# Kernel tuning notes

Measured on AMD Instinct MI355X. Metric: run time of the kernel, lower is better.

## Reference

```python
import jax, jax.numpy as jnp
import numpy as np

T, B, D = 2048, 32, 1024
AH, H = 128, 8
N, N2 = D // H, AH // H


def setup_inputs() -> dict:
    key = jax.random.key(0)
    ks = jax.random.split(key, 7)
    s1 = 1.0 / np.sqrt(N)
    s2 = 1.0 / np.sqrt(N2)
    return {
        "hyp": jax.random.normal(ks[0], (T, B, D), dtype=jnp.float32),
        "W_w": jax.random.uniform(ks[1], (N2, N), jnp.float32, -s1, s1),
        "W_b": jax.random.uniform(ks[2], (N2,), jnp.float32, -s1, s1),
        "Wm_w": jax.random.uniform(ks[3], (N2, N), jnp.float32, -s1, s1),
        "Wm_b": jax.random.uniform(ks[4], (N2,), jnp.float32, -s1, s1),
        "Wh_w": jax.random.uniform(ks[5], (1, N2), jnp.float32, -s2, s2),
        "Wh_b": jax.random.uniform(ks[6], (1,), jnp.float32, -s2, s2),
        "dan_hidden_size": D,
        "attention_hidden_size": AH,
        "multihead_size": H,
    }


def reference(hyp, W_w, W_b, Wm_w, Wm_b, Wh_w, Wh_b,
              dan_hidden_size, attention_hidden_size, multihead_size):
    t, b, d = hyp.shape
    h_ = multihead_size
    n = d // h_
    # (T,B,D) -> (B,H,T,N); weights are shared across heads in the original loop
    x = jnp.transpose(hyp.reshape(t, b, h_, n), (1, 2, 0, 3))
    m = x.mean(axis=2, keepdims=True)                      # (B,H,1,N) mean over time
    gate_x = jnp.tanh(jnp.einsum('bhtn,kn->bhtk', x, W_w) + W_b)
    gate_m = jnp.tanh(jnp.einsum('bhtn,kn->bhtk', m, Wm_w) + Wm_b)
    hgate = gate_x * gate_m                                 # (B,H,T,N2)
    logits = jnp.einsum('bhtk,ok->bhto', hgate, Wh_w) + Wh_b  # (B,H,T,1)
    a = jax.nn.softmax(logits, axis=2)                      # softmax over time
    c = jnp.sum(a * x, axis=2)                              # (B,H,N)
    return c.reshape(b, h_ * n)
```

## Files before the change

kernel.cpp:

```cpp
#include <hip/hip_runtime.h>
#include <hip/hip_fp16.h>
#include <math.h>

#define T_   2048
#define B_   32
#define D_   1024
#define H_   8
#define N_   128
#define NK   16
#define TSPL 8
#define TBLK (T_/TSPL)
#define BD4  (B_*D_/4)
#define APS  132
#define LOG2E 1.4426950408889634f

typedef __attribute__((ext_vector_type(8))) _Float16 half8;
typedef __attribute__((ext_vector_type(4))) float f32x4;

__device__ __forceinline__ half8 to_half8(float4 a, float4 b) {
    half8 r;
    r[0] = (_Float16)a.x; r[1] = (_Float16)a.y;
    r[2] = (_Float16)a.z; r[3] = (_Float16)a.w;
    r[4] = (_Float16)b.x; r[5] = (_Float16)b.y;
    r[6] = (_Float16)b.z; r[7] = (_Float16)b.w;
    return r;
}

__device__ __forceinline__ float tanh_fast(float d) {
    return 1.f - 2.f * __frcp_rn(exp2f(d * (2.f * LOG2E)) + 1.f);
}

#define LOADX(dst, step_) { \
    const int trow_ = t0 + (step_) * 64 + w * 16 + kk; \
    const size_t rb_ = (size_t)trow_ * BD4 + base4; \
    (dst)[0] = hyp4[rb_ + g * 2];      (dst)[1] = hyp4[rb_ + g * 2 + 1]; \
    (dst)[2] = hyp4[rb_ + 8 + g * 2];  (dst)[3] = hyp4[rb_ + 8 + g * 2 + 1]; \
    (dst)[4] = hyp4[rb_ + 16 + g * 2]; (dst)[5] = hyp4[rb_ + 16 + g * 2 + 1]; \
    (dst)[6] = hyp4[rb_ + 24 + g * 2]; (dst)[7] = hyp4[rb_ + 24 + g * 2 + 1]; }

__global__ __launch_bounds__(256, 4) void k_p(const float* __restrict__ hyp,
                                              const float* __restrict__ Ww,
                                              const float* __restrict__ Wb,
                                              float* __restrict__ part,
                                              __half* __restrict__ Pbuf) {
    __shared__ float red[4 * N_];
    __shared__ __half Pl[TBLK * NK];
    const int tid  = threadIdx.x;
    const int lane = tid & 63;
    const int w    = tid >> 6;
    const int blk  = blockIdx.x;
    const int bh   = blk >> 3;
    const int spl  = blk & 7;
    const int b = bh >> 3, h = bh & 7;
    const int t0 = spl * TBLK;
    const float4* hyp4 = (const float4*)hyp;
    const float4* Ww4  = (const float4*)Ww;
    const int base4 = b * (D_ / 4) + h * (N_ / 4);
    const int kk = lane & 15;
    const int g  = lane >> 4;

    half8 wf[4];
#pragma unroll
    for (int ks = 0; ks < 4; ++ks) {
        float4 wa  = Ww4[kk * 32 + ks * 8 + g * 2];
        float4 wb4 = Ww4[kk * 32 + ks * 8 + g * 2 + 1];
        wf[ks] = to_half8(wa, wb4);
    }
    const float wbr = Wb[kk];

    float4 cs[8];
#pragma unroll
    for (int m = 0; m < 8; ++m) cs[m] = make_float4(0.f, 0.f, 0.f, 0.f);

#pragma unroll
    for (int step = 0; step < 4; ++step) {
        float4 xq[8];
        LOADX(xq, step);
#pragma unroll
        for (int m = 0; m < 8; ++m) {
            cs[m].x += xq[m].x; cs[m].y += xq[m].y;
            cs[m].z += xq[m].z; cs[m].w += xq[m].w;
        }
        f32x4 acc = {0.f, 0.f, 0.f, 0.f};
#pragma unroll
        for (int ks = 0; ks < 4; ++ks) {
            half8 xf = to_half8(xq[2*ks], xq[2*ks+1]);
            acc = __builtin_amdgcn_mfma_f32_16x16x32_f16(xf, wf[ks], acc, 0, 0, 0);
        }
        const int tl = step * 64 + w * 16 + g * 4;
#pragma unroll
        for (int i = 0; i < 4; ++i)
            Pl[(tl + i) * NK + kk] = __float2half(tanh_fast(acc[i] + wbr));
    }
    __syncthreads();
    {
        const uint4* src = (const uint4*)Pl;
        uint4* dst = (uint4*)(Pbuf + ((size_t)bh * T_ + t0) * NK);
        dst[tid]       = src[tid];
        dst[tid + 256] = src[tid + 256];
    }
#pragma unroll
    for (int m = 0; m < 8; ++m) {
#pragma unroll
        for (int mask = 1; mask <= 8; mask <<= 1) {
            cs[m].x += __shfl_xor(cs[m].x, mask, 64);
            cs[m].y += __shfl_xor(cs[m].y, mask, 64);
            cs[m].z += __shfl_xor(cs[m].z, mask, 64);
            cs[m].w += __shfl_xor(cs[m].w, mask, 64);
        }
    }
    if (kk == 0) {
#pragma unroll
        for (int m = 0; m < 8; ++m) {
            int nb = 32 * (m >> 1) + 8 * g + 4 * (m & 1);
            red[w * N_ + nb + 0] = cs[m].x;
            red[w * N_ + nb + 1] = cs[m].y;
            red[w * N_ + nb + 2] = cs[m].z;
            red[w * N_ + nb + 3] = cs[m].w;
        }
    }
    __syncthreads();
    if (tid < N_)
        part[blk * N_ + tid] = (red[tid] + red[N_ + tid])
                             + (red[2*N_ + tid] + red[3*N_ + tid]);
}

__global__ __launch_bounds__(256, 4) void k_att(const float* __restrict__ hyp,
                                                const float* __restrict__ part,
                                                const float* __restrict__ Wmw,
                                                const float* __restrict__ Wmb,
                                                const float* __restrict__ Whw,
                                                const __half* __restrict__ Pbuf,
                                                float* __restrict__ attp) {
    __shared__ float m_l[N_];
    __shared__ float gw_l[NK];
    __shared__ float wexp_l[TBLK];
    __shared__ float4 red4[8][32];
    __shared__ float zred[4];
    const int tid  = threadIdx.x;
    const int lane = tid & 63;
    const int w    = tid >> 6;
    const int j    = (int)blockIdx.x;
    const int blk  = (j & 7) + 8 * (255 - (j >> 3));
    const int bh   = blk >> 3;
    const int spl  = blk & 7;
    const int b = bh >> 3, h = bh & 7;
    const int t0 = spl * TBLK;
    const float4* hyp4 = (const float4*)hyp;
    const int base4 = b * (D_ / 4) + h * (N_ / 4);

    if (tid < N_) {
        float s = 0.f;
#pragma unroll
        for (int s8 = 0; s8 < TSPL; ++s8) s += part[(bh * TSPL + s8) * N_ + tid];
        m_l[tid] = s * (1.f / (float)T_);
    }
    __syncthreads();
    if (tid < N_) {
        int k = tid >> 3, g3 = tid & 7;
        float dsum = 0.f;
#pragma unroll
        for (int i = 0; i < 16; ++i) {
            int n = g3 * 16 + i;
            dsum = fmaf(m_l[n], Wmw[k * N_ + n], dsum);
        }
        dsum += __shfl_xor(dsum, 1, 64);
        dsum += __shfl_xor(dsum, 2, 64);
        dsum += __shfl_xor(dsum, 4, 64);
        if (g3 == 0) gw_l[k] = tanhf(dsum + Wmb[k]) * Whw[k];
    }
    __syncthreads();

    {
        const uint4* pv = (const uint4*)(Pbuf + ((size_t)bh * T_ + t0) * NK);
        union { uint4 u; __half2 hh[4]; } Pa, Pb;
        Pa.u = pv[2 * tid];
        Pb.u = pv[2 * tid + 1];
        float lg = 0.f;
#pragma unroll
        for (int q = 0; q < 4; ++q) {
            float2 f0 = __half22float2(Pa.hh[q]);
            float2 f1 = __half22float2(Pb.hh[q]);
            lg = fmaf(f0.x, gw_l[2*q + 0], lg);
            lg = fmaf(f0.y, gw_l[2*q + 1], lg);
            lg = fmaf(f1.x, gw_l[8 + 2*q + 0], lg);
            lg = fmaf(f1.y, gw_l[8 + 2*q + 1], lg);
        }
        float e = exp2f(lg * LOG2E);
        wexp_l[tid] = e;
        float z = e;
        z += __shfl_xor(z, 1, 64);  z += __shfl_xor(z, 2, 64);
        z += __shfl_xor(z, 4, 64);  z += __shfl_xor(z, 8, 64);
        z += __shfl_xor(z, 16, 64); z += __shfl_xor(z, 32, 64);
        if (lane == 0) zred[w] = z;
    }
    __syncthreads();

    const int col4 = tid & 31, tg = tid >> 5;
    float4 c0 = {0.f,0.f,0.f,0.f}, c1 = {0.f,0.f,0.f,0.f};
    const float* we = &wexp_l[tg * 32];
    const size_t rbase = (size_t)(t0 + tg * 32) * BD4 + base4 + col4;
#pragma unroll
    for (int i = 0; i < 32; i += 2) {
        float w0 = we[i], w1 = we[i + 1];
        float4 x0 = hyp4[rbase + (size_t)i * BD4];
        float4 x1 = hyp4[rbase + (size_t)(i + 1) * BD4];
        c0.x = fmaf(w0, x0.x, c0.x); c0.y = fmaf(w0, x0.y, c0.y);
        c0.z = fmaf(w0, x0.z, c0.z); c0.w = fmaf(w0, x0.w, c0.w);
        c1.x = fmaf(w1, x1.x, c1.x); c1.y = fmaf(w1, x1.y, c1.y);
        c1.z = fmaf(w1, x1.z, c1.z); c1.w = fmaf(w1, x1.w, c1.w);
    }
    c0.x += c1.x; c0.y += c1.y; c0.z += c1.z; c0.w += c1.w;
    red4[tg][col4] = c0;
    __syncthreads();
    if (tid < 32) {
        float4 s = {0.f,0.f,0.f,0.f};
#pragma unroll
        for (int gg = 0; gg < 8; ++gg) {
            float4 v = red4[gg][tid];
            s.x += v.x; s.y += v.y; s.z += v.z; s.w += v.w;
        }
        *(float4*)&attp[(size_t)blk * APS + tid * 4] = s;
    } else if (tid == 32) {
        attp[(size_t)blk * APS + N_] =
            (zred[0] + zred[1]) + (zred[2] + zred[3]);
    }
}

__global__ __launch_bounds__(128) void k_red(const float* __restrict__ attp,
                                             float* __restrict__ out) {
    int bh = blockIdx.x, tid = threadIdx.x;
    float Z = 0.f, c = 0.f;
#pragma unroll
    for (int s = 0; s < TSPL; ++s) {
        const float* pp = &attp[(size_t)(bh * TSPL + s) * APS];
        Z += pp[N_];
        c += pp[tid];
    }
    out[bh * N_ + tid] = c / Z;
}

extern "C" void kernel_launch(void* const* d_in, const int* in_sizes, int n_in,
                              void* d_out, int out_size, void* d_ws, size_t ws_size,
                              hipStream_t stream) {
    const float* hyp = (const float*)d_in[0];
    const float* Ww  = (const float*)d_in[1];
    const float* Wb  = (const float*)d_in[2];
    const float* Wmw = (const float*)d_in[3];
    const float* Wmb = (const float*)d_in[4];
    const float* Whw = (const float*)d_in[5];
    float* out  = (float*)d_out;
    float* part = (float*)d_ws;
    float* attp = part + 2048 * N_;
    __half* Pbuf = (__half*)((char*)d_ws + (4 << 20));

    k_p  <<<dim3(B_ * H_ * TSPL), 256, 0, stream>>>(hyp, Ww, Wb, part, Pbuf);
    k_att<<<dim3(B_ * H_ * TSPL), 256, 0, stream>>>(hyp, part, Wmw, Wmb, Whw,
                                                    Pbuf, attp);
    k_red<<<dim3(B_ * H_), 128, 0, stream>>>(attp, out);
}
```

Baseline: 108.1 us.

## Stash fp16 copy of x in k_p and read it in attention pass

While streaming hyp, the projection kernel now writes an fp16 copy of each head's x rows into workspace, laid out contiguously per (b,h). The attention kernel reads that half-size copy for the weighted sum instead of re-reading the fp32 input. The hyp loads become nontemporal, and the reversed block order that favoured cache reuse is removed. This trades a second full fp32 read for a half-size write plus a half-size read, and it lowers the precision of the weighted sum of x.

```diff
diff --git a/kernel.cpp b/kernel.cpp
--- a/kernel.cpp
+++ b/kernel.cpp
@@ -17,7 +17,7 @@
 typedef __attribute__((ext_vector_type(8))) _Float16 half8;
 typedef __attribute__((ext_vector_type(4))) float f32x4;
 
-__device__ __forceinline__ half8 to_half8(float4 a, float4 b) {
+__device__ __forceinline__ half8 to_half8(f32x4 a, f32x4 b) {
     half8 r;
     r[0] = (_Float16)a.x; r[1] = (_Float16)a.y;
     r[2] = (_Float16)a.z; r[3] = (_Float16)a.w;
@@ -30,19 +30,24 @@
     return 1.f - 2.f * __frcp_rn(exp2f(d * (2.f * LOG2E)) + 1.f);
 }
 
-#define LOADX(dst, step_) { \
+#define LOADX_NT(dst, step_) { \
     const int trow_ = t0 + (step_) * 64 + w * 16 + kk; \
     const size_t rb_ = (size_t)trow_ * BD4 + base4; \
-    (dst)[0] = hyp4[rb_ + g * 2];      (dst)[1] = hyp4[rb_ + g * 2 + 1]; \
-    (dst)[2] = hyp4[rb_ + 8 + g * 2];  (dst)[3] = hyp4[rb_ + 8 + g * 2 + 1]; \
-    (dst)[4] = hyp4[rb_ + 16 + g * 2]; (dst)[5] = hyp4[rb_ + 16 + g * 2 + 1]; \
-    (dst)[6] = hyp4[rb_ + 24 + g * 2]; (dst)[7] = hyp4[rb_ + 24 + g * 2 + 1]; }
+    (dst)[0] = __builtin_nontemporal_load(&hyp4n[rb_ + g * 2]); \
+    (dst)[1] = __builtin_nontemporal_load(&hyp4n[rb_ + g * 2 + 1]); \
+    (dst)[2] = __builtin_nontemporal_load(&hyp4n[rb_ + 8 + g * 2]); \
+    (dst)[3] = __builtin_nontemporal_load(&hyp4n[rb_ + 8 + g * 2 + 1]); \
+    (dst)[4] = __builtin_nontemporal_load(&hyp4n[rb_ + 16 + g * 2]); \
+    (dst)[5] = __builtin_nontemporal_load(&hyp4n[rb_ + 16 + g * 2 + 1]); \
+    (dst)[6] = __builtin_nontemporal_load(&hyp4n[rb_ + 24 + g * 2]); \
+    (dst)[7] = __builtin_nontemporal_load(&hyp4n[rb_ + 24 + g * 2 + 1]); }
 
 __global__ __launch_bounds__(256, 4) void k_p(const float* __restrict__ hyp,
                                               const float* __restrict__ Ww,
                                               const float* __restrict__ Wb,
                                               float* __restrict__ part,
-                                              __half* __restrict__ Pbuf) {
+                                              __half* __restrict__ Pbuf,
+                                              __half* __restrict__ xcb) {
     __shared__ float red[4 * N_];
     __shared__ __half Pl[TBLK * NK];
     const int tid  = threadIdx.x;
@@ -53,8 +58,8 @@
     const int spl  = blk & 7;
     const int b = bh >> 3, h = bh & 7;
     const int t0 = spl * TBLK;
-    const float4* hyp4 = (const float4*)hyp;
-    const float4* Ww4  = (const float4*)Ww;
+    const f32x4* hyp4n = (const f32x4*)hyp;
+    const f32x4* Ww4   = (const f32x4*)Ww;
     const int base4 = b * (D_ / 4) + h * (N_ / 4);
     const int kk = lane & 15;
     const int g  = lane >> 4;
@@ -62,20 +67,22 @@
     half8 wf[4];
 #pragma unroll
     for (int ks = 0; ks < 4; ++ks) {
-        float4 wa  = Ww4[kk * 32 + ks * 8 + g * 2];
-        float4 wb4 = Ww4[kk * 32 + ks * 8 + g * 2 + 1];
+        f32x4 wa  = Ww4[kk * 32 + ks * 8 + g * 2];
+        f32x4 wb4 = Ww4[kk * 32 + ks * 8 + g * 2 + 1];
         wf[ks] = to_half8(wa, wb4);
     }
     const float wbr = Wb[kk];
 
-    float4 cs[8];
-#pragma unroll
-    for (int m = 0; m < 8; ++m) cs[m] = make_float4(0.f, 0.f, 0.f, 0.f);
+    f32x4 cs[8];
+#pragma unroll
+    for (int m = 0; m < 8; ++m) cs[m] = (f32x4){0.f, 0.f, 0.f, 0.f};
 
 #pragma unroll
     for (int step = 0; step < 4; ++step) {
-        float4 xq[8];
-        LOADX(xq, step);
+        f32x4 xq[8];
+        LOADX_NT(xq, step);
+        const int trow = t0 + step * 64 + w * 16 + kk;
+        __half* xrow = xcb + ((size_t)bh * T_ + trow) * N_;
 #pragma unroll
         for (int m = 0; m < 8; ++m) {
             cs[m].x += xq[m].x; cs[m].y += xq[m].y;
@@ -86,6 +93,7 @@
         for (int ks = 0; ks < 4; ++ks) {
             half8 xf = to_half8(xq[2*ks], xq[2*ks+1]);
             acc = __builtin_amdgcn_mfma_f32_16x16x32_f16(xf, wf[ks], acc, 0, 0, 0);
+            *(half8*)&xrow[ks * 32 + g * 8] = xf;
         }
         const int tl = step * 64 + w * 16 + g * 4;
 #pragma unroll
@@ -125,7 +133,7 @@
                              + (red[2*N_ + tid] + red[3*N_ + tid]);
 }
 
-__global__ __launch_bounds__(256, 4) void k_att(const float* __restrict__ hyp,
+__global__ __launch_bounds__(256, 4) void k_att(const __half* __restrict__ xcb,
                                                 const float* __restrict__ part,
                                                 const float* __restrict__ Wmw,
                                                 const float* __restrict__ Wmb,
@@ -135,19 +143,15 @@
     __shared__ float m_l[N_];
     __shared__ float gw_l[NK];
     __shared__ float wexp_l[TBLK];
-    __shared__ float4 red4[8][32];
+    __shared__ float4 redc[16][16][2];
     __shared__ float zred[4];
     const int tid  = threadIdx.x;
     const int lane = tid & 63;
     const int w    = tid >> 6;
-    const int j    = (int)blockIdx.x;
-    const int blk  = (j & 7) + 8 * (255 - (j >> 3));
+    const int blk  = (int)blockIdx.x;
     const int bh   = blk >> 3;
     const int spl  = blk & 7;
-    const int b = bh >> 3, h = bh & 7;
     const int t0 = spl * TBLK;
-    const float4* hyp4 = (const float4*)hyp;
-    const int base4 = b * (D_ / 4) + h * (N_ / 4);
 
     if (tid < N_) {
         float s = 0.f;
@@ -196,32 +200,37 @@
     }
     __syncthreads();
 
-    const int col4 = tid & 31, tg = tid >> 5;
+    const int c8 = tid & 15, tg = tid >> 4;
     float4 c0 = {0.f,0.f,0.f,0.f}, c1 = {0.f,0.f,0.f,0.f};
-    const float* we = &wexp_l[tg * 32];
-    const size_t rbase = (size_t)(t0 + tg * 32) * BD4 + base4 + col4;
-#pragma unroll
-    for (int i = 0; i < 32; i += 2) {
-        float w0 = we[i], w1 = we[i + 1];
-        float4 x0 = hyp4[rbase + (size_t)i * BD4];
-        float4 x1 = hyp4[rbase + (size_t)(i + 1) * BD4];
-        c0.x = fmaf(w0, x0.x, c0.x); c0.y = fmaf(w0, x0.y, c0.y);
-        c0.z = fmaf(w0, x0.z, c0.z); c0.w = fmaf(w0, x0.w, c0.w);
-        c1.x = fmaf(w1, x1.x, c1.x); c1.y = fmaf(w1, x1.y, c1.y);
-        c1.z = fmaf(w1, x1.z, c1.z); c1.w = fmaf(w1, x1.w, c1.w);
-    }
-    c0.x += c1.x; c0.y += c1.y; c0.z += c1.z; c0.w += c1.w;
-    red4[tg][col4] = c0;
-    __syncthreads();
-    if (tid < 32) {
-        float4 s = {0.f,0.f,0.f,0.f};
-#pragma unroll
-        for (int gg = 0; gg < 8; ++gg) {
-            float4 v = red4[gg][tid];
-            s.x += v.x; s.y += v.y; s.z += v.z; s.w += v.w;
-        }
-        *(float4*)&attp[(size_t)blk * APS + tid * 4] = s;
-    } else if (tid == 32) {
+    const float* we = &wexp_l[tg * 16];
+    const __half* xr = xcb + ((size_t)bh * T_ + t0 + tg * 16) * N_ + c8 * 8;
+#pragma unroll
+    for (int i = 0; i < 16; ++i) {
+        union { uint4 u; __half2 hh[4]; } X;
+        X.u = *(const uint4*)(xr + (size_t)i * N_);
+        float e = we[i];
+        float2 f0 = __half22float2(X.hh[0]);
+        float2 f1 = __half22float2(X.hh[1]);
+        float2 f2 = __half22float2(X.hh[2]);
+        float2 f3 = __half22float2(X.hh[3]);
+        c0.x = fmaf(e, f0.x, c0.x); c0.y = fmaf(e, f0.y, c0.y);
+        c0.z = fmaf(e, f1.x, c0.z); c0.w = fmaf(e, f1.y, c0.w);
+        c1.x = fmaf(e, f2.x, c1.x); c1.y = fmaf(e, f2.y, c1.y);
+        c1.z = fmaf(e, f3.x, c1.z); c1.w = fmaf(e, f3.y, c1.w);
+    }
+    redc[tg][c8][0] = c0;
+    redc[tg][c8][1] = c1;
+    __syncthreads();
+    if (tid < N_) {
+        int cc8 = tid >> 3, jj = tid & 7;
+        float s = 0.f;
+#pragma unroll
+        for (int g16 = 0; g16 < 16; ++g16) {
+            const float* rr = (const float*)&redc[g16][cc8][0];
+            s += rr[jj];
+        }
+        attp[(size_t)blk * APS + tid] = s;
+    } else if (tid == N_) {
         attp[(size_t)blk * APS + N_] =
             (zred[0] + zred[1]) + (zred[2] + zred[3]);
     }
@@ -253,9 +262,11 @@
     float* part = (float*)d_ws;
     float* attp = part + 2048 * N_;
     __half* Pbuf = (__half*)((char*)d_ws + (4 << 20));
-
-    k_p  <<<dim3(B_ * H_ * TSPL), 256, 0, stream>>>(hyp, Ww, Wb, part, Pbuf);
-    k_att<<<dim3(B_ * H_ * TSPL), 256, 0, stream>>>(hyp, part, Wmw, Wmb, Whw,
+    __half* xcb  = (__half*)((char*)d_ws + (24 << 20));
+
+    k_p  <<<dim3(B_ * H_ * TSPL), 256, 0, stream>>>(hyp, Ww, Wb, part, Pbuf,
+                                                    xcb);
+    k_att<<<dim3(B_ * H_ * TSPL), 256, 0, stream>>>(xcb, part, Wmw, Wmb, Whw,
                                                     Pbuf, attp);
     k_red<<<dim3(B_ * H_), 128, 0, stream>>>(attp, out);
 }
```

Result: slower. 143.6 us (+32.8%).

## Fuse three kernels into one 1024-thread block per batch-head

Applied to the files above, without the earlier changes.

Replaces the three-kernel pipeline (partial mean + gate projection, attention, final reduction) with a single kernel in which one 1024-thread block handles a whole (batch, head) pair across all 2048 timesteps. The gate values and softmax weights stay in shared memory, so the global Pbuf and partial-sum round trips and two kernel launches disappear. In exchange the grid shrinks from 2048 blocks to 256, which may underfill the GPU. Each block also needs a large shared-memory footprint, limiting occupancy while the memory-bound second pass over hyp runs.

```diff
diff --git a/kernel.cpp b/kernel.cpp
--- a/kernel.cpp
+++ b/kernel.cpp
@@ -8,16 +8,13 @@
 #define H_   8
 #define N_   128
 #define NK   16
-#define TSPL 8
-#define TBLK (T_/TSPL)
 #define BD4  (B_*D_/4)
-#define APS  132
 #define LOG2E 1.4426950408889634f
 
 typedef __attribute__((ext_vector_type(8))) _Float16 half8;
 typedef __attribute__((ext_vector_type(4))) float f32x4;
 
-__device__ __forceinline__ half8 to_half8(float4 a, float4 b) {
+__device__ __forceinline__ half8 to_half8(f32x4 a, f32x4 b) {
     half8 r;
     r[0] = (_Float16)a.x; r[1] = (_Float16)a.y;
     r[2] = (_Float16)a.z; r[3] = (_Float16)a.w;
@@ -30,31 +27,26 @@
     return 1.f - 2.f * __frcp_rn(exp2f(d * (2.f * LOG2E)) + 1.f);
 }
 
-#define LOADX(dst, step_) { \
-    const int trow_ = t0 + (step_) * 64 + w * 16 + kk; \
-    const size_t rb_ = (size_t)trow_ * BD4 + base4; \
-    (dst)[0] = hyp4[rb_ + g * 2];      (dst)[1] = hyp4[rb_ + g * 2 + 1]; \
-    (dst)[2] = hyp4[rb_ + 8 + g * 2];  (dst)[3] = hyp4[rb_ + 8 + g * 2 + 1]; \
-    (dst)[4] = hyp4[rb_ + 16 + g * 2]; (dst)[5] = hyp4[rb_ + 16 + g * 2 + 1]; \
-    (dst)[6] = hyp4[rb_ + 24 + g * 2]; (dst)[7] = hyp4[rb_ + 24 + g * 2 + 1]; }
-
-__global__ __launch_bounds__(256, 4) void k_p(const float* __restrict__ hyp,
-                                              const float* __restrict__ Ww,
-                                              const float* __restrict__ Wb,
-                                              float* __restrict__ part,
-                                              __half* __restrict__ Pbuf) {
-    __shared__ float red[4 * N_];
-    __shared__ __half Pl[TBLK * NK];
+__global__ __launch_bounds__(1024, 4) void k_fused(
+        const float* __restrict__ hyp,  const float* __restrict__ Ww,
+        const float* __restrict__ Wb,   const float* __restrict__ Wmw,
+        const float* __restrict__ Wmb,  const float* __restrict__ Whw,
+        float* __restrict__ out) {
+    __shared__ __align__(16) __half Pl[T_ * NK];
+    __shared__ __align__(16) float scratch[4096];
+    __shared__ float wexp_l[T_];
+    __shared__ float m_l[N_];
+    __shared__ float gw_l[NK];
+    __shared__ float zred[16];
+    __shared__ float zfin_s;
+
     const int tid  = threadIdx.x;
     const int lane = tid & 63;
     const int w    = tid >> 6;
-    const int blk  = blockIdx.x;
-    const int bh   = blk >> 3;
-    const int spl  = blk & 7;
+    const int bh   = blockIdx.x;
     const int b = bh >> 3, h = bh & 7;
-    const int t0 = spl * TBLK;
-    const float4* hyp4 = (const float4*)hyp;
-    const float4* Ww4  = (const float4*)Ww;
+    const f32x4* hyp4n = (const f32x4*)hyp;
+    const f32x4* Ww4   = (const f32x4*)Ww;
     const int base4 = b * (D_ / 4) + h * (N_ / 4);
     const int kk = lane & 15;
     const int g  = lane >> 4;
@@ -62,20 +54,26 @@
     half8 wf[4];
 #pragma unroll
     for (int ks = 0; ks < 4; ++ks) {
-        float4 wa  = Ww4[kk * 32 + ks * 8 + g * 2];
-        float4 wb4 = Ww4[kk * 32 + ks * 8 + g * 2 + 1];
+        f32x4 wa  = Ww4[kk * 32 + ks * 8 + g * 2];
+        f32x4 wb4 = Ww4[kk * 32 + ks * 8 + g * 2 + 1];
         wf[ks] = to_half8(wa, wb4);
     }
     const float wbr = Wb[kk];
 
-    float4 cs[8];
-#pragma unroll
-    for (int m = 0; m < 8; ++m) cs[m] = make_float4(0.f, 0.f, 0.f, 0.f);
-
-#pragma unroll
-    for (int step = 0; step < 4; ++step) {
-        float4 xq[8];
-        LOADX(xq, step);
+    f32x4 cs[8];
+#pragma unroll
+    for (int m = 0; m < 8; ++m) cs[m] = (f32x4){0.f, 0.f, 0.f, 0.f};
+
+#pragma unroll
+    for (int s = 0; s < 8; ++s) {
+        const int tb = w * 128 + s * 16;
+        const int trow = tb + kk;
+        const size_t rb = (size_t)trow * BD4 + base4;
+        f32x4 xq[8];
+        xq[0] = hyp4n[rb + g * 2];      xq[1] = hyp4n[rb + g * 2 + 1];
+        xq[2] = hyp4n[rb + 8 + g * 2];  xq[3] = hyp4n[rb + 8 + g * 2 + 1];
+        xq[4] = hyp4n[rb + 16 + g * 2]; xq[5] = hyp4n[rb + 16 + g * 2 + 1];
+        xq[6] = hyp4n[rb + 24 + g * 2]; xq[7] = hyp4n[rb + 24 + g * 2 + 1];
 #pragma unroll
         for (int m = 0; m < 8; ++m) {
             cs[m].x += xq[m].x; cs[m].y += xq[m].y;
@@ -87,17 +85,10 @@
             half8 xf = to_half8(xq[2*ks], xq[2*ks+1]);
             acc = __builtin_amdgcn_mfma_f32_16x16x32_f16(xf, wf[ks], acc, 0, 0, 0);
         }
-        const int tl = step * 64 + w * 16 + g * 4;
+        const int tl = tb + g * 4;
 #pragma unroll
         for (int i = 0; i < 4; ++i)
             Pl[(tl + i) * NK + kk] = __float2half(tanh_fast(acc[i] + wbr));
-    }
-    __syncthreads();
-    {
-        const uint4* src = (const uint4*)Pl;
-        uint4* dst = (uint4*)(Pbuf + ((size_t)bh * T_ + t0) * NK);
-        dst[tid]       = src[tid];
-        dst[tid + 256] = src[tid + 256];
     }
 #pragma unroll
     for (int m = 0; m < 8; ++m) {
@@ -113,46 +104,17 @@
 #pragma unroll
         for (int m = 0; m < 8; ++m) {
             int nb = 32 * (m >> 1) + 8 * g + 4 * (m & 1);
-            red[w * N_ + nb + 0] = cs[m].x;
-            red[w * N_ + nb + 1] = cs[m].y;
-            red[w * N_ + nb + 2] = cs[m].z;
-            red[w * N_ + nb + 3] = cs[m].w;
-        }
-    }
-    __syncthreads();
-    if (tid < N_)
-        part[blk * N_ + tid] = (red[tid] + red[N_ + tid])
-                             + (red[2*N_ + tid] + red[3*N_ + tid]);
-}
-
-__global__ __launch_bounds__(256, 4) void k_att(const float* __restrict__ hyp,
-                                                const float* __restrict__ part,
-                                                const float* __restrict__ Wmw,
-                                                const float* __restrict__ Wmb,
-                                                const float* __restrict__ Whw,
-                                                const __half* __restrict__ Pbuf,
-                                                float* __restrict__ attp) {
-    __shared__ float m_l[N_];
-    __shared__ float gw_l[NK];
-    __shared__ float wexp_l[TBLK];
-    __shared__ float4 red4[8][32];
-    __shared__ float zred[4];
-    const int tid  = threadIdx.x;
-    const int lane = tid & 63;
-    const int w    = tid >> 6;
-    const int j    = (int)blockIdx.x;
-    const int blk  = (j & 7) + 8 * (255 - (j >> 3));
-    const int bh   = blk >> 3;
-    const int spl  = blk & 7;
-    const int b = bh >> 3, h = bh & 7;
-    const int t0 = spl * TBLK;
-    const float4* hyp4 = (const float4*)hyp;
-    const int base4 = b * (D_ / 4) + h * (N_ / 4);
-
+            scratch[w * N_ + nb + 0] = cs[m].x;
+            scratch[w * N_ + nb + 1] = cs[m].y;
+            scratch[w * N_ + nb + 2] = cs[m].z;
+            scratch[w * N_ + nb + 3] = cs[m].w;
+        }
+    }
+    __syncthreads();
     if (tid < N_) {
         float s = 0.f;
 #pragma unroll
-        for (int s8 = 0; s8 < TSPL; ++s8) s += part[(bh * TSPL + s8) * N_ + tid];
+        for (int ww = 0; ww < 16; ++ww) s += scratch[ww * N_ + tid];
         m_l[tid] = s * (1.f / (float)T_);
     }
     __syncthreads();
@@ -172,72 +134,66 @@
     __syncthreads();
 
     {
-        const uint4* pv = (const uint4*)(Pbuf + ((size_t)bh * T_ + t0) * NK);
-        union { uint4 u; __half2 hh[4]; } Pa, Pb;
-        Pa.u = pv[2 * tid];
-        Pb.u = pv[2 * tid + 1];
-        float lg = 0.f;
-#pragma unroll
-        for (int q = 0; q < 4; ++q) {
-            float2 f0 = __half22float2(Pa.hh[q]);
-            float2 f1 = __half22float2(Pb.hh[q]);
-            lg = fmaf(f0.x, gw_l[2*q + 0], lg);
-            lg = fmaf(f0.y, gw_l[2*q + 1], lg);
-            lg = fmaf(f1.x, gw_l[8 + 2*q + 0], lg);
-            lg = fmaf(f1.y, gw_l[8 + 2*q + 1], lg);
-        }
-        float e = exp2f(lg * LOG2E);
-        wexp_l[tid] = e;
-        float z = e;
-        z += __shfl_xor(z, 1, 64);  z += __shfl_xor(z, 2, 64);
-        z += __shfl_xor(z, 4, 64);  z += __shfl_xor(z, 8, 64);
-        z += __shfl_xor(z, 16, 64); z += __shfl_xor(z, 32, 64);
-        if (lane == 0) zred[w] = z;
-    }
-    __syncthreads();
+        float zl = 0.f;
+#pragma unroll
+        for (int r = 0; r < 2; ++r) {
+            const int t = r * 1024 + tid;
+            const uint4* pv = (const uint4*)&Pl[t * NK];
+            union { uint4 u; __half2 hh[4]; } Pa, Pb;
+            Pa.u = pv[0]; Pb.u = pv[1];
+            float lg = 0.f;
+#pragma unroll
+            for (int q = 0; q < 4; ++q) {
+                float2 f0 = __half22float2(Pa.hh[q]);
+                float2 f1 = __half22float2(Pb.hh[q]);
+                lg = fmaf(f0.x, gw_l[2*q + 0], lg);
+                lg = fmaf(f0.y, gw_l[2*q + 1], lg);
+                lg = fmaf(f1.x, gw_l[8 + 2*q + 0], lg);
+                lg = fmaf(f1.y, gw_l[8 + 2*q + 1], lg);
+            }
+            float e = exp2f(lg * LOG2E);
+            wexp_l[t] = e;
+            zl += e;
+        }
+        zl += __shfl_xor(zl, 1, 64);  zl += __shfl_xor(zl, 2, 64);
+        zl += __shfl_xor(zl, 4, 64);  zl += __shfl_xor(zl, 8, 64);
+        zl += __shfl_xor(zl, 16, 64); zl += __shfl_xor(zl, 32, 64);
+        if (lane == 0) zred[w] = zl;
+    }
+    __syncthreads();
+    if (tid == 0) {
+        float z = 0.f;
+#pragma unroll
+        for (int i = 0; i < 16; ++i) z += zred[i];
+        zfin_s = z;
+    }
 
     const int col4 = tid & 31, tg = tid >> 5;
-    float4 c0 = {0.f,0.f,0.f,0.f}, c1 = {0.f,0.f,0.f,0.f};
-    const float* we = &wexp_l[tg * 32];
-    const size_t rbase = (size_t)(t0 + tg * 32) * BD4 + base4 + col4;
-#pragma unroll
-    for (int i = 0; i < 32; i += 2) {
+    f32x4 c0 = {0.f,0.f,0.f,0.f}, c1 = {0.f,0.f,0.f,0.f};
+    const float* we = &wexp_l[tg * 64];
+    const size_t rbase = (size_t)(tg * 64) * BD4 + base4 + col4;
+#pragma unroll 8
+    for (int i = 0; i < 64; i += 2) {
         float w0 = we[i], w1 = we[i + 1];
-        float4 x0 = hyp4[rbase + (size_t)i * BD4];
-        float4 x1 = hyp4[rbase + (size_t)(i + 1) * BD4];
+        f32x4 x0 = hyp4n[rbase + (size_t)i * BD4];
+        f32x4 x1 = hyp4n[rbase + (size_t)(i + 1) * BD4];
         c0.x = fmaf(w0, x0.x, c0.x); c0.y = fmaf(w0, x0.y, c0.y);
         c0.z = fmaf(w0, x0.z, c0.z); c0.w = fmaf(w0, x0.w, c0.w);
         c1.x = fmaf(w1, x1.x, c1.x); c1.y = fmaf(w1, x1.y, c1.y);
         c1.z = fmaf(w1, x1.z, c1.z); c1.w = fmaf(w1, x1.w, c1.w);
     }
     c0.x += c1.x; c0.y += c1.y; c0.z += c1.z; c0.w += c1.w;
-    red4[tg][col4] = c0;
-    __syncthreads();
-    if (tid < 32) {
-        float4 s = {0.f,0.f,0.f,0.f};
-#pragma unroll
-        for (int gg = 0; gg < 8; ++gg) {
-            float4 v = red4[gg][tid];
-            s.x += v.x; s.y += v.y; s.z += v.z; s.w += v.w;
-        }
-        *(float4*)&attp[(size_t)blk * APS + tid * 4] = s;
-    } else if (tid == 32) {
-        attp[(size_t)blk * APS + N_] =
-            (zred[0] + zred[1]) + (zred[2] + zred[3]);
-    }
-}
-
-__global__ __launch_bounds__(128) void k_red(const float* __restrict__ attp,
-                                             float* __restrict__ out) {
-    int bh = blockIdx.x, tid = threadIdx.x;
-    float Z = 0.f, c = 0.f;
-#pragma unroll
-    for (int s = 0; s < TSPL; ++s) {
-        const float* pp = &attp[(size_t)(bh * TSPL + s) * APS];
-        Z += pp[N_];
-        c += pp[tid];
-    }
-    out[bh * N_ + tid] = c / Z;
+    __syncthreads();
+    *(f32x4*)&scratch[(tg * 32 + col4) * 4] = c0;
+    __syncthreads();
+    if (tid < N_) {
+        const int c4 = tid >> 2, jj = tid & 3;
+        float s = 0.f;
+#pragma unroll
+        for (int t32 = 0; t32 < 32; ++t32)
+            s += scratch[(t32 * 32 + c4) * 4 + jj];
+        out[bh * N_ + tid] = s / zfin_s;
+    }
 }
 
 extern "C" void kernel_launch(void* const* d_in, const int* in_sizes, int n_in,
@@ -249,13 +205,7 @@
     const float* Wmw = (const float*)d_in[3];
     const float* Wmb = (const float*)d_in[4];
     const float* Whw = (const float*)d_in[5];
-    float* out  = (float*)d_out;
-    float* part = (float*)d_ws;
-    float* attp = part + 2048 * N_;
-    __half* Pbuf = (__half*)((char*)d_ws + (4 << 20));
-
-    k_p  <<<dim3(B_ * H_ * TSPL), 256, 0, stream>>>(hyp, Ww, Wb, part, Pbuf);
-    k_att<<<dim3(B_ * H_ * TSPL), 256, 0, stream>>>(hyp, part, Wmw, Wmb, Whw,
-                                                    Pbuf, attp);
-    k_red<<<dim3(B_ * H_), 128, 0, stream>>>(attp, out);
-}
+    float* out = (float*)d_out;
+
+    k_fused<<<dim3(B_ * H_), 1024, 0, stream>>>(hyp, Ww, Wb, Wmw, Wmb, Whw, out);
+}
```

New measurement: 168.8 us. 56.1% more time.
